# Performance work log

Measured on AMD Instinct MI355X. Metric: run time of the kernel, lower is better.

The kernel has to match this reference:

```python
import jax, jax.numpy as jnp
import numpy as np

VOCAB = 50000
CUTOFF = [20000, 40000]
EMBED_DIM = 1024
FACTOR = 4.0
PAD = 1


def setup_inputs() -> dict:
    key = jax.random.key(0)
    k0, k1, k2, k3, k4, k5 = jax.random.split(key, 6)
    ends = [0] + CUTOFF + [VOCAB]
    dims = [int(EMBED_DIM // FACTOR ** i) for i in range(len(ends) - 1)]  # [1024, 256, 64]
    sizes = [ends[i + 1] - ends[i] for i in range(len(ends) - 1)]          # [20000, 20000, 10000]
    input_ids = jax.random.randint(k0, (8, 4096), 0, VOCAB, dtype=jnp.int32)
    # nn.Embedding default init: N(0, 1)
    emb0 = jax.random.normal(k1, (sizes[0], dims[0]), dtype=jnp.float32)
    emb1 = jax.random.normal(k2, (sizes[1], dims[1]), dtype=jnp.float32)
    emb2 = jax.random.normal(k3, (sizes[2], dims[2]), dtype=jnp.float32)
    # projection weight [embedding_dim, dim_i], init N(0, dim_i^-0.5)
    proj1 = jax.random.normal(k4, (EMBED_DIM, dims[1]), dtype=jnp.float32) * dims[1] ** -0.5
    proj2 = jax.random.normal(k5, (EMBED_DIM, dims[2]), dtype=jnp.float32) * dims[2] ** -0.5
    return {"input_ids": input_ids, "emb0": emb0, "emb1": emb1, "emb2": emb2,
            "proj1": proj1, "proj2": proj2}


def reference(input_ids, emb0, emb1, emb2, proj1, proj2):
    ends = [0] + CUTOFF + [VOCAB]
    tables = [emb0, emb1, emb2]
    projs = [None, proj1, proj2]
    result = jnp.zeros(input_ids.shape + (EMBED_DIM,), dtype=emb0.dtype)
    for i, (tab, proj) in enumerate(zip(tables, projs)):
        l, r = ends[i], ends[i + 1]
        # padding_idx zeroes the local pad row of each cluster table
        tab = tab.at[PAD].set(0.0)
        local = jnp.clip(input_ids - l, 0, r - l - 1)  # safe gather index
        e = tab[local]                                  # [B, S, dim_i]
        if proj is not None:
            e = jnp.einsum('bsd,ed->bse', e, proj)      # Linear(dim_i -> EMBED_DIM), no bias
        in_cluster = ((input_ids >= l) & (input_ids < r))[..., None]
        result = jnp.where(in_cluster, e, result)
    return result
```

## Files before the change

kernel.cpp:

```cpp
#include <hip/hip_runtime.h>


constexpr int NTOK = 8 * 4096;
constexpr int C1 = 20000;
constexpr int C2 = 40000;
constexpr int DIM = 1024;
constexpr int PAD = 1;
constexpr int K1 = 256, K2 = 64;
constexpr int NP1 = DIM * K1;
constexpr int NP2 = DIM * K2;
constexpr int GTOK = 32;
constexpr int NB1 = NTOK / GTOK;
constexpr int NB2 = NTOK / GTOK;

typedef unsigned short u16;
typedef unsigned int u32;
typedef unsigned long long u64;
typedef __attribute__((ext_vector_type(8))) short bf16x8;
typedef __attribute__((ext_vector_type(4))) float f32x4;

__device__ __forceinline__ u16 f2bf(float f) {
    u32 u = __builtin_bit_cast(u32, f);
    return (u16)((u + 0x7FFFu + ((u >> 16) & 1u)) >> 16);
}

__device__ __forceinline__ void nt_store4(const float4& v, float4* p) {
    f32x4 w = {v.x, v.y, v.z, v.w};
    __builtin_nontemporal_store(w, (f32x4*)p);
}

template<int K>
__device__ __forceinline__ void cvt_body(int idx, const float* __restrict__ src,
                                         u16* __restrict__ dst) {
    constexpr int KS = K / 32;
    int lane = idx & 63;
    int rest = idx >> 6;
    int kstep = rest % KS;
    int ntile = rest / KS;
    int n = ntile * 16 + (lane & 15);
    int k = kstep * 32 + (lane >> 4) * 8;
    const float4* p = (const float4*)(src + (size_t)n * K + k);
    float4 a = p[0], b = p[1];
    u16 t[8] = {f2bf(a.x), f2bf(a.y), f2bf(a.z), f2bf(a.w),
                f2bf(b.x), f2bf(b.y), f2bf(b.z), f2bf(b.w)};
    *(int4*)(dst + (size_t)idx * 8) = *(const int4*)t;
}

__global__ __launch_bounds__(512) void prep_k(const int* __restrict__ ids,
        u16* __restrict__ list1, u16* __restrict__ list2, int* __restrict__ counters,
        const float* __restrict__ proj1, const float* __restrict__ proj2,
        u16* __restrict__ projL1, u16* __restrict__ projL2) {
    int b = blockIdx.x;
    int tid = threadIdx.x;
    if (b >= 64) {
        if (b < 128) cvt_body<K1>((b - 64) * 512 + tid, proj1, projL1);
        else         cvt_body<K2>((b - 128) * 512 + tid, proj2, projL2);
        return;
    }
    __shared__ int woff1[8], woff2[8];
    __shared__ int base1, base2;
    int i = b * 512 + tid;
    int id = ids[i];
    bool in1 = (id >= C1) & (id < C2);
    bool in2 = (id >= C2);
    u64 b1 = __ballot(in1);
    u64 b2 = __ballot(in2);
    int wave = tid >> 6, lane = tid & 63;
    if (lane == 0) { woff1[wave] = __popcll(b1); woff2[wave] = __popcll(b2); }
    __syncthreads();
    if (tid == 0) {
        int t1 = 0, t2 = 0;
        #pragma unroll
        for (int w = 0; w < 8; ++w) {
            int c1 = woff1[w]; woff1[w] = t1; t1 += c1;
            int c2 = woff2[w]; woff2[w] = t2; t2 += c2;
        }
        base1 = atomicAdd(&counters[0], t1);
        base2 = atomicAdd(&counters[16], t2);
    }
    __syncthreads();
    u64 lt = (lane == 63) ? ~0ull >> 1 : (1ull << lane) - 1;
    if (in1) list1[base1 + woff1[wave] + __popcll(b1 & lt)] = (u16)i;
    if (in2) list2[base2 + woff2[wave] + __popcll(b2 & lt)] = (u16)i;
}

template<int K>
__device__ __forceinline__ void gemm_body(int b, const int* __restrict__ ids,
        const float* __restrict__ emb, const u16* __restrict__ projL,
        const u16* __restrict__ list, const int* __restrict__ count_ptr,
        int base, float* __restrict__ out,
        u16* __restrict__ A, u16* __restrict__ s_tok, int* __restrict__ s_loc) {
    constexpr int K8 = K / 8;
    constexpr int KS = K / 32;
    constexpr int LROW = K + 8;
    int count = *count_ptr;
    int t0 = b * GTOK;
    if (t0 >= count) return;
    int nt_valid = min(GTOK, count - t0);
    int tid = threadIdx.x;

    if (tid < GTOK) {
        int tokidx = 0, loc = -1;
        if (tid < nt_valid) {
            tokidx = list[t0 + tid];
            loc = ids[tokidx] - base;
            if (loc == PAD) loc = -1;
        }
        s_tok[tid] = (u16)tokidx;
        s_loc[tid] = loc;
    }
    __syncthreads();

    for (int c = tid; c < GTOK * K8; c += 512) {
        int m = c / K8, k8 = c % K8;
        int loc = s_loc[m];
        float4 v0 = make_float4(0.f,0.f,0.f,0.f), v1 = v0;
        if (loc >= 0) {
            const float4* p = (const float4*)(emb + (size_t)loc * K) + k8 * 2;
            v0 = p[0]; v1 = p[1];
        }
        u16 t[8] = {f2bf(v0.x), f2bf(v0.y), f2bf(v0.z), f2bf(v0.w),
                    f2bf(v1.x), f2bf(v1.y), f2bf(v1.z), f2bf(v1.w)};
        *(int4*)&A[m * LROW + k8 * 8] = *(const int4*)t;
    }
    __syncthreads();

    int wave = tid >> 6;
    int lane = tid & 63;
    int lr = lane & 15;
    int lk = (lane >> 4) * 8;
    const bf16x8* Bfrag = (const bf16x8*)projL;

    f32x4 acc[2][8] = {};
    for (int ks = 0; ks < KS; ++ks) {
        bf16x8 a0 = *(const bf16x8*)&A[lr * LROW + ks * 32 + lk];
        bf16x8 a1 = *(const bf16x8*)&A[(16 + lr) * LROW + ks * 32 + lk];
        #pragma unroll
        for (int nt = 0; nt < 8; ++nt) {
            bf16x8 bb = Bfrag[((size_t)((wave * 8 + nt) * KS + ks)) * 64 + lane];
            acc[0][nt] = __builtin_amdgcn_mfma_f32_16x16x32_bf16(a0, bb, acc[0][nt], 0, 0, 0);
            acc[1][nt] = __builtin_amdgcn_mfma_f32_16x16x32_bf16(a1, bb, acc[1][nt], 0, 0, 0);
        }
    }

    int nb = wave * 128;
    int rbase = (lane >> 4) * 4;
    #pragma unroll
    for (int mt = 0; mt < 2; ++mt) {
        #pragma unroll
        for (int r = 0; r < 4; ++r) {
            int trow = mt * 16 + rbase + r;
            if (trow < nt_valid) {
                float* orow = out + (size_t)s_tok[trow] * DIM + nb + lr;
                #pragma unroll
                for (int nt = 0; nt < 8; ++nt)
                    __builtin_nontemporal_store(acc[mt][nt][r], &orow[nt * 16]);
            }
        }
    }
}

__global__ __launch_bounds__(512, 4) void fused_k(const int* __restrict__ ids,
        const float* __restrict__ emb0, const float* __restrict__ emb1,
        const float* __restrict__ emb2, const u16* __restrict__ projL1,
        const u16* __restrict__ projL2, const u16* __restrict__ list1,
        const u16* __restrict__ list2, const int* __restrict__ counters,
        float* __restrict__ out) {
    __shared__ __align__(16) u16 A[GTOK * (K1 + 8)];
    __shared__ u16 s_tok[GTOK];
    __shared__ int s_loc[GTOK];
    int b = blockIdx.x;
    int stripe = b / 6;
    int role = b % 6;
    if (role == 0) {
        gemm_body<K1>(stripe, ids, emb1, projL1, list1, &counters[0], C1, out, A, s_tok, s_loc);
        return;
    }
    if (role == 1) {
        gemm_body<K2>(stripe, ids, emb2, projL2, list2, &counters[16], C2, out, A, s_tok, s_loc);
        return;
    }
    int cb = stripe * 4 + (role - 2);
    int tbase = cb * 8;
    int tid = threadIdx.x;
    const float4* e4 = (const float4*)emb0;
    float4* o4 = (float4*)out;
    #pragma unroll
    for (int r = 0; r < 4; ++r) {
        int j = r * 512 + tid;
        int tok = tbase + (j >> 8);
        int d4 = j & 255;
        int id = ids[tok];
        if (id < C1) {
            float4 v = make_float4(0.f, 0.f, 0.f, 0.f);
            if (id != PAD) v = e4[(size_t)id * 256 + d4];
            nt_store4(v, &o4[(size_t)tok * 256 + d4]);
        }
    }
}

extern "C" void kernel_launch(void* const* d_in, const int* in_sizes, int n_in,
                              void* d_out, int out_size, void* d_ws, size_t ws_size,
                              hipStream_t stream) {
    const int*   ids   = (const int*)d_in[0];
    const float* emb0  = (const float*)d_in[1];
    const float* emb1  = (const float*)d_in[2];
    const float* emb2  = (const float*)d_in[3];
    const float* proj1 = (const float*)d_in[4];
    const float* proj2 = (const float*)d_in[5];
    float* out = (float*)d_out;

    int* counters = (int*)d_ws;
    u16* list1  = (u16*)((char*)d_ws + 128);
    u16* list2  = list1 + NTOK;
    u16* projL1 = list2 + NTOK;
    u16* projL2 = projL1 + NP1;

    hipMemsetAsync(d_ws, 0, 128, stream);
    prep_k<<<144, 512, 0, stream>>>(ids, list1, list2, counters,
                                    proj1, proj2, projL1, projL2);
    fused_k<<<NB1 * 6, 512, 0, stream>>>(ids, emb0, emb1, emb2,
                                         projL1, projL2, list1, list2,
                                         counters, out);
}
```

Baseline: 64.29 us.

## Shrink GEMM token tile to 16 with 256-thread blocks and wider per-wave N

Halves the token group per GEMM block to 16 and cuts blocks to 256 threads (4 waves), so each wave now covers 256 output columns with 16 accumulators. All B fragments for a k-step are loaded before the MFMAs are issued. The grid is reorganised into 4 roles per stripe, and the plain gather path now has each thread copy one float4 per token across 8 tokens. GEMM output stores drop the nontemporal hint. The aim is more, smaller blocks for better load balance, at the cost of reading the projection weights twice as often per token and higher register pressure.

```diff
diff --git a/kernel.cpp b/kernel.cpp
--- a/kernel.cpp
+++ b/kernel.cpp
@@ -9,9 +9,8 @@
 constexpr int K1 = 256, K2 = 64;
 constexpr int NP1 = DIM * K1;
 constexpr int NP2 = DIM * K2;
-constexpr int GTOK = 32;
-constexpr int NB1 = NTOK / GTOK;
-constexpr int NB2 = NTOK / GTOK;
+constexpr int GTOK = 16;
+constexpr int NSTRIPE = NTOK / GTOK;
 
 typedef unsigned short u16;
 typedef unsigned int u32;
@@ -111,7 +110,7 @@
     }
     __syncthreads();
 
-    for (int c = tid; c < GTOK * K8; c += 512) {
+    for (int c = tid; c < GTOK * K8; c += 256) {
         int m = c / K8, k8 = c % K8;
         int loc = s_loc[m];
         float4 v0 = make_float4(0.f,0.f,0.f,0.f), v1 = v0;
@@ -131,36 +130,32 @@
     int lk = (lane >> 4) * 8;
     const bf16x8* Bfrag = (const bf16x8*)projL;
 
-    f32x4 acc[2][8] = {};
+    f32x4 acc[16] = {};
     for (int ks = 0; ks < KS; ++ks) {
         bf16x8 a0 = *(const bf16x8*)&A[lr * LROW + ks * 32 + lk];
-        bf16x8 a1 = *(const bf16x8*)&A[(16 + lr) * LROW + ks * 32 + lk];
+        bf16x8 bb[16];
         #pragma unroll
-        for (int nt = 0; nt < 8; ++nt) {
-            bf16x8 bb = Bfrag[((size_t)((wave * 8 + nt) * KS + ks)) * 64 + lane];
-            acc[0][nt] = __builtin_amdgcn_mfma_f32_16x16x32_bf16(a0, bb, acc[0][nt], 0, 0, 0);
-            acc[1][nt] = __builtin_amdgcn_mfma_f32_16x16x32_bf16(a1, bb, acc[1][nt], 0, 0, 0);
-        }
-    }
-
-    int nb = wave * 128;
+        for (int nt = 0; nt < 16; ++nt)
+            bb[nt] = Bfrag[((size_t)((wave * 16 + nt) * KS + ks)) * 64 + lane];
+        #pragma unroll
+        for (int nt = 0; nt < 16; ++nt)
+            acc[nt] = __builtin_amdgcn_mfma_f32_16x16x32_bf16(a0, bb[nt], acc[nt], 0, 0, 0);
+    }
+
     int rbase = (lane >> 4) * 4;
     #pragma unroll
-    for (int mt = 0; mt < 2; ++mt) {
-        #pragma unroll
-        for (int r = 0; r < 4; ++r) {
-            int trow = mt * 16 + rbase + r;
-            if (trow < nt_valid) {
-                float* orow = out + (size_t)s_tok[trow] * DIM + nb + lr;
-                #pragma unroll
-                for (int nt = 0; nt < 8; ++nt)
-                    __builtin_nontemporal_store(acc[mt][nt][r], &orow[nt * 16]);
-            }
-        }
-    }
-}
-
-__global__ __launch_bounds__(512, 4) void fused_k(const int* __restrict__ ids,
+    for (int r = 0; r < 4; ++r) {
+        int trow = rbase + r;
+        if (trow < nt_valid) {
+            float* orow = out + (size_t)s_tok[trow] * DIM + wave * 256 + lr;
+            #pragma unroll
+            for (int nt = 0; nt < 16; ++nt)
+                orow[nt * 16] = acc[nt][r];
+        }
+    }
+}
+
+__global__ __launch_bounds__(256, 4) void fused_k(const int* __restrict__ ids,
         const float* __restrict__ emb0, const float* __restrict__ emb1,
         const float* __restrict__ emb2, const u16* __restrict__ projL1,
         const u16* __restrict__ projL2, const u16* __restrict__ list1,
@@ -170,8 +165,8 @@
     __shared__ u16 s_tok[GTOK];
     __shared__ int s_loc[GTOK];
     int b = blockIdx.x;
-    int stripe = b / 6;
-    int role = b % 6;
+    int stripe = b >> 2;
+    int role = b & 3;
     if (role == 0) {
         gemm_body<K1>(stripe, ids, emb1, projL1, list1, &counters[0], C1, out, A, s_tok, s_loc);
         return;
@@ -180,21 +175,18 @@
         gemm_body<K2>(stripe, ids, emb2, projL2, list2, &counters[16], C2, out, A, s_tok, s_loc);
         return;
     }
-    int cb = stripe * 4 + (role - 2);
-    int tbase = cb * 8;
+    int tbase = (stripe * 2 + (role - 2)) * 8;
     int tid = threadIdx.x;
     const float4* e4 = (const float4*)emb0;
     float4* o4 = (float4*)out;
     #pragma unroll
-    for (int r = 0; r < 4; ++r) {
-        int j = r * 512 + tid;
-        int tok = tbase + (j >> 8);
-        int d4 = j & 255;
+    for (int r = 0; r < 8; ++r) {
+        int tok = tbase + r;
         int id = ids[tok];
         if (id < C1) {
             float4 v = make_float4(0.f, 0.f, 0.f, 0.f);
-            if (id != PAD) v = e4[(size_t)id * 256 + d4];
-            nt_store4(v, &o4[(size_t)tok * 256 + d4]);
+            if (id != PAD) v = e4[(size_t)id * 256 + tid];
+            nt_store4(v, &o4[(size_t)tok * 256 + tid]);
         }
     }
 }
@@ -219,7 +211,7 @@
     hipMemsetAsync(d_ws, 0, 128, stream);
     prep_k<<<144, 512, 0, stream>>>(ids, list1, list2, counters,
                                     proj1, proj2, projL1, projL2);
-    fused_k<<<NB1 * 6, 512, 0, stream>>>(ids, emb0, emb1, emb2,
-                                         projL1, projL2, list1, list2,
-                                         counters, out);
-}
+    fused_k<<<NSTRIPE * 4, 256, 0, stream>>>(ids, emb0, emb1, emb2,
+                                             projL1, projL2, list1, list2,
+                                             counters, out);
+}
```

Measured after the change: 91.68 us. +42.6%, slower.
